# Kernel tuning notes

Measured on AMD Instinct MI355X. Metric: run time of the kernel, lower is better.

## Reference

```python
import jax, jax.numpy as jnp
import numpy as np

DECAY = 0.8
COMMITMENT = 1.0
EPS = 1e-05


def setup_inputs() -> dict:
    key = jax.random.key(0)
    k1, k2, k3 = jax.random.split(key, 3)
    dim, n_embed = 256, 8192
    input = jax.random.normal(k1, (8, 2048, dim), dtype=jnp.float32)
    embed = jax.random.normal(k2, (dim, n_embed), dtype=jnp.float32)
    cluster_size = jnp.zeros((n_embed,), dtype=jnp.float32)
    embed_avg = jax.random.normal(k3, (dim, n_embed), dtype=jnp.float32)
    return {"input": input, "embed": embed, "cluster_size": cluster_size, "embed_avg": embed_avg}


def reference(input, embed, cluster_size, embed_avg):
    dim, n_embed = embed.shape
    flatten = input.reshape(-1, dim)  # [N, d]
    dist = (jnp.sum(flatten * flatten, axis=1, keepdims=True)
            - 2.0 * flatten @ embed
            + jnp.sum(embed * embed, axis=0, keepdims=True))  # [N, C]
    embed_ind_flat = jnp.argmin(dist, axis=1)  # [N]
    embed_ind = embed_ind_flat.reshape(input.shape[:-1])
    quantize = jnp.take(embed.T, embed_ind_flat, axis=0).reshape(input.shape)

    # training-mode EMA codebook update (onehot.sum(0) and x^T @ onehot as segment ops)
    counts = jax.ops.segment_sum(jnp.ones_like(embed_ind_flat, dtype=input.dtype),
                                 embed_ind_flat, num_segments=n_embed)  # [C]
    embed_sum = jax.ops.segment_sum(flatten, embed_ind_flat, num_segments=n_embed).T  # [d, C]
    new_cluster_size = cluster_size * DECAY + counts * (1.0 - DECAY)
    new_embed_avg = embed_avg * DECAY + embed_sum * (1.0 - DECAY)
    smoothed = (new_cluster_size + EPS) / (jnp.sum(new_cluster_size) + n_embed * EPS)
    smoothed = smoothed * jnp.sum(new_cluster_size)
    new_embed = new_embed_avg / smoothed[None, :]

    commit_loss = jnp.mean((quantize - input) ** 2) * COMMITMENT
    # straight-through (no grad here in fwd-only, values identical)
    quantize_st = input + jax.lax.stop_gradient(quantize - input)
    return quantize_st, embed_ind, commit_loss, new_embed, new_cluster_size, new_embed_avg
```

## Files before the change

### kernel.cpp

```cpp
#include <hip/hip_runtime.h>
#include <hip/hip_bf16.h>
#include <float.h>
#include <stdint.h>

#define N_ROWS 16384
#define DIM 256
#define NE 8192
#define K2 768
#define DECAY 0.8f
#define OMD 0.2f
#define EPS 1e-5f
#define NPAN 8
#define NKT 24
#define NVT 96

#define WS_X2     0
#define WS_EMBEDT 0
#define WS_ESUMT  2097152
#define WS_B2T    6291456
#define WS_ENORM  9437184
#define WS_COUNTS 9445376
#define WS_SMOOTH 9453568
#define WS_PI     9592832
#define WS_LOSS   9740288
#define WS_TOTAL  9740289

#define OUT_Q    0
#define OUT_IND  4194304
#define OUT_LOSS 4210688
#define OUT_NE   4210689
#define OUT_NCS  6307841
#define OUT_NEA  6316033

typedef __attribute__((ext_vector_type(8))) short bf16x8;
typedef __attribute__((ext_vector_type(4))) float f32x4;

static __device__ __forceinline__ ushort f2bf(float f) {
    uint32_t u = __float_as_uint(f);
    uint32_t r = (u + 0x7fffu + ((u >> 16) & 1u)) >> 16;
    return (ushort)r;
}
static __device__ __forceinline__ float bf2f(ushort h) {
    return __uint_as_float(((uint32_t)h) << 16);
}
static __device__ __forceinline__ void async16(void* lds, const void* g) {
    __builtin_amdgcn_global_load_lds(
        (const __attribute__((address_space(1))) uint32_t*)g,
        (__attribute__((address_space(3))) uint32_t*)lds, 16, 0, 0);
}

__global__ __launch_bounds__(256) void convx_kernel(const float* __restrict__ x,
                                                    ushort* __restrict__ X2) {
    int i = blockIdx.x * 256 + threadIdx.x;
    int row = i >> 6, q = (i & 63) * 4;
    float4 v = *(const float4*)&x[(size_t)row * 256 + q];
    ushort4 hi, lo;
    hi.x = f2bf(v.x); hi.y = f2bf(v.y); hi.z = f2bf(v.z); hi.w = f2bf(v.w);
    lo.x = f2bf(v.x - bf2f(hi.x)); lo.y = f2bf(v.y - bf2f(hi.y));
    lo.z = f2bf(v.z - bf2f(hi.z)); lo.w = f2bf(v.w - bf2f(hi.w));
    *(ushort4*)&X2[(size_t)row * K2 + q]       = hi;
    *(ushort4*)&X2[(size_t)row * K2 + 256 + q] = lo;
    *(ushort4*)&X2[(size_t)row * K2 + 512 + q] = hi;
}

__global__ __launch_bounds__(256) void prepB_kernel(const float* __restrict__ embed,
                                                    ushort* __restrict__ B2T,
                                                    float* __restrict__ enorm) {
    __shared__ float t[32][33];
    int c0 = blockIdx.x * 32, d0 = blockIdx.y * 32;
    int tx = threadIdx.x & 31, ty = threadIdx.x >> 5;
    #pragma unroll
    for (int r = 0; r < 4; ++r)
        t[ty + r * 8][tx] = embed[(size_t)(d0 + ty + r * 8) * NE + c0 + tx];
    __syncthreads();
    #pragma unroll
    for (int r = 0; r < 4; ++r) {
        int c = c0 + ty + r * 8, d = d0 + tx;
        float v = t[tx][ty + r * 8];
        ushort hi = f2bf(v);
        ushort lo = f2bf(v - bf2f(hi));
        B2T[(size_t)c * K2 + d]       = hi;
        B2T[(size_t)c * K2 + 256 + d] = hi;
        B2T[(size_t)c * K2 + 512 + d] = lo;
        float s = v * v;
        #pragma unroll
        for (int off = 16; off; off >>= 1) s += __shfl_down(s, off, 32);
        if (tx == 0) atomicAdd(&enorm[c], s);
    }
}

__global__ __launch_bounds__(256) void transpose_kernel(const float* __restrict__ embed,
                                                        float* __restrict__ embedT) {
    __shared__ float t[32][33];
    int c0 = blockIdx.x * 32, d0 = blockIdx.y * 32;
    int tx = threadIdx.x & 31, ty = threadIdx.x >> 5;
    #pragma unroll
    for (int r = 0; r < 4; ++r)
        t[ty + r * 8][tx] = embed[(size_t)(d0 + ty + r * 8) * NE + c0 + tx];
    __syncthreads();
    #pragma unroll
    for (int r = 0; r < 4; ++r)
        embedT[(size_t)(c0 + ty + r * 8) * DIM + d0 + tx] = t[tx][ty + r * 8];
}

#define MFMA16(d, a, b) d = __builtin_amdgcn_mfma_f32_16x16x32_bf16(a, b, d, 0, 0, 0)

__global__ __launch_bounds__(1024, 4) void argmin_mfma(
    const ushort* __restrict__ X2, const ushort* __restrict__ B2T,
    const float* __restrict__ enorm, int* __restrict__ pi) {
    __shared__ ushort smem[55296];
    float* const redv = (float*)(smem + 49152);
    int*   const redc = (int*)(smem + 51200);
    float* const enS  = (float*)(smem + 53248);

    const int lin = blockIdx.x;
    const int by = lin & 7, bx = lin >> 3;
    const int row0 = bx * 256, colb = by * 1024;

    const int tid = threadIdx.x;
    const int lane = tid & 63, wid = tid >> 6;
    const int fl = lane & 15, fh = lane >> 4;
    const int wr = wid >> 2, wc = wid & 3;

    enS[tid] = enorm[colb + tid];
    redv[tid] = FLT_MAX; redc[tid] = 0x7fffffff;

    const int srow = tid >> 2;
    const int swz = (tid & 3) ^ ((tid >> 3) & 3);
    const size_t aBase = (size_t)(row0 + srow) * K2 + swz * 8;
    const size_t bBase = (size_t)(colb + srow) * K2 + swz * 8;

    async16(smem + 0 * 8192 + tid * 8, X2 + aBase);
    async16(smem + 24576 + 0 * 8192 + tid * 8, B2T + bBase);
    async16(smem + 1 * 8192 + tid * 8, X2 + aBase + 32);
    async16(smem + 24576 + 1 * 8192 + tid * 8, B2T + bBase + 32);

    const int xo = (fh ^ ((fl >> 1) & 3)) * 8;
    int aOff[4], bOff[4];
    #pragma unroll
    for (int m = 0; m < 4; ++m) aOff[m] = (wr * 64 + m * 16 + fl) * 32 + xo;
    #pragma unroll
    for (int n = 0; n < 4; ++n) bOff[n] = (wc * 64 + n * 16 + fl) * 32 + xo;

    f32x4 acc[4][4];
    #pragma unroll
    for (int m = 0; m < 4; ++m)
        #pragma unroll
        for (int n = 0; n < 4; ++n) acc[m][n] = (f32x4){0.f, 0.f, 0.f, 0.f};

    int cur = 0;
    #pragma unroll 1
    for (int vt = 0; vt < NVT; ++vt) {
        const int t = vt % NKT;
        int nv2 = vt + 2; if (nv2 >= NVT) nv2 -= NVT;
        const int nt2 = nv2 % NKT, nct2 = nv2 / NKT;
        int nbuf = cur + 2; if (nbuf >= 3) nbuf -= 3;

        async16(smem + nbuf * 8192 + tid * 8, X2 + aBase + (size_t)nt2 * 32);
        async16(smem + 24576 + nbuf * 8192 + tid * 8,
                B2T + bBase + (size_t)nct2 * 196608 + (size_t)nt2 * 32);

        asm volatile("s_waitcnt vmcnt(4)" ::: "memory");
        __builtin_amdgcn_s_barrier();
        __builtin_amdgcn_sched_barrier(0);

        const ushort* Ac = smem + cur * 8192;
        const ushort* Bc = smem + 24576 + cur * 8192;
        bf16x8 af[4], bf[4];
        #pragma unroll
        for (int n = 0; n < 4; ++n) bf[n] = *(const bf16x8*)&Bc[bOff[n]];
        #pragma unroll
        for (int m = 0; m < 4; ++m) af[m] = *(const bf16x8*)&Ac[aOff[m]];

        __builtin_amdgcn_s_setprio(1);
        #pragma unroll
        for (int m = 0; m < 4; ++m)
            #pragma unroll
            for (int n = 0; n < 4; ++n)
                MFMA16(acc[m][n], af[m], bf[n]);
        __builtin_amdgcn_s_setprio(0);

        if (t == NKT - 1) {
            const int ct = vt / NKT;
            const int cb = colb + ct * 256 + wc * 64;
            float en[4];
            #pragma unroll
            for (int n = 0; n < 4; ++n) en[n] = enS[ct * 256 + wc * 64 + n * 16 + fl];
            #pragma unroll
            for (int m = 0; m < 4; ++m)
                #pragma unroll
                for (int r = 0; r < 4; ++r) {
                    float bv = FLT_MAX; int bc = 0x7fffffff;
                    #pragma unroll
                    for (int n = 0; n < 4; ++n) {
                        float s = __builtin_fmaf(-2.f, acc[m][n][r], en[n]);
                        int c = cb + n * 16 + fl;
                        if (s < bv) { bv = s; bc = c; }
                    }
                    #pragma unroll
                    for (int off = 1; off < 16; off <<= 1) {
                        float ov = __shfl_xor(bv, off, 64);
                        int oc = __shfl_xor(bc, off, 64);
                        if (ov < bv || (ov == bv && oc < bc)) { bv = ov; bc = oc; }
                    }
                    if (fl == 0) {
                        const int slot = (wr * 64 + m * 16 + fh * 4 + r) * 4 + wc;
                        float cv = redv[slot]; int cc = redc[slot];
                        if (bv < cv || (bv == cv && bc < cc)) {
                            redv[slot] = bv; redc[slot] = bc;
                        }
                    }
                }
            #pragma unroll
            for (int m = 0; m < 4; ++m)
                #pragma unroll
                for (int n = 0; n < 4; ++n) acc[m][n] = (f32x4){0.f, 0.f, 0.f, 0.f};
        }
        __builtin_amdgcn_s_barrier();
        __builtin_amdgcn_sched_barrier(0);
        cur = cur + 1 == 3 ? 0 : cur + 1;
    }

    asm volatile("s_waitcnt vmcnt(0) lgkmcnt(0)" ::: "memory");
    __builtin_amdgcn_s_barrier();
    if (tid < 256) {
        float bv = redv[tid * 4]; int bc = redc[tid * 4];
        #pragma unroll
        for (int w = 1; w < 4; ++w) {
            float v = redv[tid * 4 + w]; int c = redc[tid * 4 + w];
            if (v < bv || (v == bv && c < bc)) { bv = v; bc = c; }
        }
        pi[(size_t)(row0 + tid) * NPAN + by] = bc;
    }
}

__global__ __launch_bounds__(256) void rerank_gather(
    const float* __restrict__ x, const float* __restrict__ embedT,
    const int* __restrict__ pi, float* __restrict__ out_ind,
    float* __restrict__ q_out, float* __restrict__ esumT,
    float* __restrict__ counts, float* __restrict__ loss_acc) {
    const int row = blockIdx.x * 4 + (threadIdx.x >> 6);
    const int lane = threadIdx.x & 63;
    float4 xv = *(const float4*)&x[(size_t)row * DIM + lane * 4];
    float bestd = FLT_MAX; int besti = 0;
    float4 ebest = {0.f, 0.f, 0.f, 0.f};
    #pragma unroll
    for (int p = 0; p < NPAN; ++p) {
        const int c = pi[(size_t)row * NPAN + p];
        float4 e = *(const float4*)&embedT[(size_t)c * DIM + lane * 4];
        float dx = e.x - xv.x, dy = e.y - xv.y, dz = e.z - xv.z, dw = e.w - xv.w;
        float s = dx * dx + dy * dy + dz * dz + dw * dw;
        #pragma unroll
        for (int off = 32; off; off >>= 1) s += __shfl_down(s, off);
        s = __shfl(s, 0);
        if (s < bestd) { bestd = s; besti = c; ebest = e; }
    }
    *(float4*)&q_out[(size_t)row * DIM + lane * 4] = ebest;
    __shared__ float ls[4];
    if (lane == 0) {
        out_ind[row] = (float)besti;
        ls[threadIdx.x >> 6] = bestd;
        atomicAdd(&counts[besti], 1.0f);
    }
    atomicAdd(&esumT[(size_t)besti * DIM + lane * 4 + 0], xv.x);
    atomicAdd(&esumT[(size_t)besti * DIM + lane * 4 + 1], xv.y);
    atomicAdd(&esumT[(size_t)besti * DIM + lane * 4 + 2], xv.z);
    atomicAdd(&esumT[(size_t)besti * DIM + lane * 4 + 3], xv.w);
    __syncthreads();
    if (threadIdx.x == 0) atomicAdd(loss_acc, ls[0] + ls[1] + ls[2] + ls[3]);
}

__global__ void ncs_kernel(const float* __restrict__ cs, const float* __restrict__ counts,
                           float* __restrict__ out_ncs, float* __restrict__ total) {
    int c = blockIdx.x * 256 + threadIdx.x;
    float v = cs[c] * DECAY + counts[c] * OMD;
    out_ncs[c] = v;
    float s = v;
    #pragma unroll
    for (int off = 32; off; off >>= 1) s += __shfl_down(s, off);
    __shared__ float bs[4];
    if ((threadIdx.x & 63) == 0) bs[threadIdx.x >> 6] = s;
    __syncthreads();
    if (threadIdx.x == 0) atomicAdd(total, bs[0] + bs[1] + bs[2] + bs[3]);
}

__global__ void smooth_kernel(const float* __restrict__ out_ncs, const float* __restrict__ total,
                              float* __restrict__ smoothed, const float* __restrict__ loss_acc,
                              float* __restrict__ out_loss) {
    int c = blockIdx.x * 256 + threadIdx.x;
    float tot = *total;
    float v = out_ncs[c];
    smoothed[c] = (v + EPS) / (tot + (float)NE * EPS) * tot;
    if (blockIdx.x == 0 && threadIdx.x == 0)
        *out_loss = *loss_acc * (1.0f / ((float)N_ROWS * (float)DIM));
}

__global__ __launch_bounds__(256) void final_kernel(
    const float* __restrict__ embed_avg, const float* __restrict__ esumT,
    const float* __restrict__ smoothed, float* __restrict__ out_ne,
    float* __restrict__ out_nea) {
    __shared__ float t[32][33];
    int c0 = blockIdx.x * 32, d0 = blockIdx.y * 32;
    int tx = threadIdx.x & 31, ty = threadIdx.x >> 5;
    #pragma unroll
    for (int r = 0; r < 4; ++r)
        t[ty + r * 8][tx] = esumT[(size_t)(c0 + ty + r * 8) * DIM + d0 + tx];
    __syncthreads();
    #pragma unroll
    for (int r = 0; r < 4; ++r) {
        int d = d0 + ty + r * 8, c = c0 + tx;
        float es = t[tx][ty + r * 8];
        float ea = embed_avg[(size_t)d * NE + c] * DECAY + es * OMD;
        out_nea[(size_t)d * NE + c] = ea;
        out_ne[(size_t)d * NE + c] = ea / smoothed[c];
    }
}

extern "C" void kernel_launch(void* const* d_in, const int* in_sizes, int n_in,
                              void* d_out, int out_size, void* d_ws, size_t ws_size,
                              hipStream_t stream) {
    const float* input     = (const float*)d_in[0];
    const float* embed     = (const float*)d_in[1];
    const float* cs        = (const float*)d_in[2];
    const float* embed_avg = (const float*)d_in[3];
    float* out = (float*)d_out;
    float* ws  = (float*)d_ws;

    hipMemsetAsync(ws + WS_COUNTS, 0, (size_t)8192 * 4, stream);
    hipMemsetAsync(ws + WS_ENORM, 0, (size_t)8192 * 4, stream);
    hipMemsetAsync(ws + WS_LOSS, 0, (size_t)2 * 4, stream);

    convx_kernel<<<4096, 256, 0, stream>>>(input, (ushort*)(ws + WS_X2));
    prepB_kernel<<<dim3(256, 8), 256, 0, stream>>>(embed, (ushort*)(ws + WS_B2T),
                                                   ws + WS_ENORM);
    argmin_mfma<<<512, 1024, 0, stream>>>(
        (const ushort*)(ws + WS_X2), (const ushort*)(ws + WS_B2T), ws + WS_ENORM,
        (int*)(ws + WS_PI));
    transpose_kernel<<<dim3(256, 8), 256, 0, stream>>>(embed, ws + WS_EMBEDT);
    hipMemsetAsync(ws + WS_ESUMT, 0, (size_t)2097152 * 4, stream);
    rerank_gather<<<4096, 256, 0, stream>>>(input, ws + WS_EMBEDT, (int*)(ws + WS_PI),
                                            out + OUT_IND, out + OUT_Q,
                                            ws + WS_ESUMT, ws + WS_COUNTS, ws + WS_LOSS);
    ncs_kernel<<<32, 256, 0, stream>>>(cs, ws + WS_COUNTS, out + OUT_NCS, ws + WS_TOTAL);
    smooth_kernel<<<32, 256, 0, stream>>>(out + OUT_NCS, ws + WS_TOTAL, ws + WS_SMOOTH,
                                          ws + WS_LOSS, out + OUT_LOSS);
    final_kernel<<<dim3(256, 8), 256, 0, stream>>>(embed_avg, ws + WS_ESUMT, ws + WS_SMOOTH,
                                                   out + OUT_NE, out + OUT_NEA);
}
```

Baseline: 461.0 us.

## Split argmin GEMM per 256-column tile across blocks, merge via 64-bit atomicMin

Each argmin block now handles a single 256x256 output tile instead of looping over four column tiles, so the grid is four times larger. Per-panel partial minima are combined across blocks with a packed (order-preserving float key, index) 64-bit atomicMin into a workspace array that is pre-filled with 0xFF. The pipeline drops from triple to double buffering, shared memory shrinks, and the launch bound changes to 2 blocks per CU. This is meant to raise parallelism and occupancy and to remove the in-loop epilogue branch, at the cost of global atomics, an extra memset and a shallower prefetch.

```diff
diff --git a/kernel.cpp b/kernel.cpp
--- a/kernel.cpp
+++ b/kernel.cpp
@@ -11,8 +11,7 @@
 #define OMD 0.2f
 #define EPS 1e-5f
 #define NPAN 8
-#define NKT 24
-#define NVT 96
+#define NVT 24
 
 #define WS_X2     0
 #define WS_EMBEDT 0
@@ -21,7 +20,7 @@
 #define WS_ENORM  9437184
 #define WS_COUNTS 9445376
 #define WS_SMOOTH 9453568
-#define WS_PI     9592832
+#define WS_PV64   9461760
 #define WS_LOSS   9740288
 #define WS_TOTAL  9740289
 
@@ -105,24 +104,27 @@
 
 #define MFMA16(d, a, b) d = __builtin_amdgcn_mfma_f32_16x16x32_bf16(a, b, d, 0, 0, 0)
 
-__global__ __launch_bounds__(1024, 4) void argmin_mfma(
+__global__ __launch_bounds__(1024, 2) void argmin_mfma(
     const ushort* __restrict__ X2, const ushort* __restrict__ B2T,
-    const float* __restrict__ enorm, int* __restrict__ pi) {
-    __shared__ ushort smem[55296];
-    float* const redv = (float*)(smem + 49152);
-    int*   const redc = (int*)(smem + 51200);
-    float* const enS  = (float*)(smem + 53248);
+    const float* __restrict__ enorm, unsigned long long* __restrict__ pv64) {
+    __shared__ ushort smem[37376];
+    float* const redv = (float*)(smem + 32768);
+    int*   const redc = (int*)(smem + 34816);
+    float* const enS  = (float*)(smem + 36864);
 
     const int lin = blockIdx.x;
-    const int by = lin & 7, bx = lin >> 3;
-    const int row0 = bx * 256, colb = by * 1024;
+    const int xcd = lin & 7, q = lin >> 3;
+    const int rb = q & 7, ct = q >> 3;
+    const int row0 = (xcd * 8 + rb) * 256;
+    const int colb = ct * 256;
+    const int panel = ct >> 2;
 
     const int tid = threadIdx.x;
     const int lane = tid & 63, wid = tid >> 6;
     const int fl = lane & 15, fh = lane >> 4;
     const int wr = wid >> 2, wc = wid & 3;
 
-    enS[tid] = enorm[colb + tid];
+    if (tid < 256) enS[tid] = enorm[colb + tid];
     redv[tid] = FLT_MAX; redc[tid] = 0x7fffffff;
 
     const int srow = tid >> 2;
@@ -131,9 +133,7 @@
     const size_t bBase = (size_t)(colb + srow) * K2 + swz * 8;
 
     async16(smem + 0 * 8192 + tid * 8, X2 + aBase);
-    async16(smem + 24576 + 0 * 8192 + tid * 8, B2T + bBase);
-    async16(smem + 1 * 8192 + tid * 8, X2 + aBase + 32);
-    async16(smem + 24576 + 1 * 8192 + tid * 8, B2T + bBase + 32);
+    async16(smem + 16384 + 0 * 8192 + tid * 8, B2T + bBase);
 
     const int xo = (fh ^ ((fl >> 1) & 3)) * 8;
     int aOff[4], bOff[4];
@@ -148,24 +148,20 @@
         #pragma unroll
         for (int n = 0; n < 4; ++n) acc[m][n] = (f32x4){0.f, 0.f, 0.f, 0.f};
 
-    int cur = 0;
     #pragma unroll 1
     for (int vt = 0; vt < NVT; ++vt) {
-        const int t = vt % NKT;
-        int nv2 = vt + 2; if (nv2 >= NVT) nv2 -= NVT;
-        const int nt2 = nv2 % NKT, nct2 = nv2 / NKT;
-        int nbuf = cur + 2; if (nbuf >= 3) nbuf -= 3;
-
-        async16(smem + nbuf * 8192 + tid * 8, X2 + aBase + (size_t)nt2 * 32);
-        async16(smem + 24576 + nbuf * 8192 + tid * 8,
-                B2T + bBase + (size_t)nct2 * 196608 + (size_t)nt2 * 32);
-
-        asm volatile("s_waitcnt vmcnt(4)" ::: "memory");
+        int nv = vt + 1; if (nv == NVT) nv = 0;
+        const int nbuf = nv & 1, cbuf = vt & 1;
+
+        async16(smem + nbuf * 8192 + tid * 8, X2 + aBase + (size_t)nv * 32);
+        async16(smem + 16384 + nbuf * 8192 + tid * 8, B2T + bBase + (size_t)nv * 32);
+
+        asm volatile("s_waitcnt vmcnt(2)" ::: "memory");
         __builtin_amdgcn_s_barrier();
         __builtin_amdgcn_sched_barrier(0);
 
-        const ushort* Ac = smem + cur * 8192;
-        const ushort* Bc = smem + 24576 + cur * 8192;
+        const ushort* Ac = smem + cbuf * 8192;
+        const ushort* Bc = smem + 16384 + cbuf * 8192;
         bf16x8 af[4], bf[4];
         #pragma unroll
         for (int n = 0; n < 4; ++n) bf[n] = *(const bf16x8*)&Bc[bOff[n]];
@@ -180,49 +176,36 @@
                 MFMA16(acc[m][n], af[m], bf[n]);
         __builtin_amdgcn_s_setprio(0);
 
-        if (t == NKT - 1) {
-            const int ct = vt / NKT;
-            const int cb = colb + ct * 256 + wc * 64;
-            float en[4];
-            #pragma unroll
-            for (int n = 0; n < 4; ++n) en[n] = enS[ct * 256 + wc * 64 + n * 16 + fl];
-            #pragma unroll
-            for (int m = 0; m < 4; ++m)
-                #pragma unroll
-                for (int r = 0; r < 4; ++r) {
-                    float bv = FLT_MAX; int bc = 0x7fffffff;
-                    #pragma unroll
-                    for (int n = 0; n < 4; ++n) {
-                        float s = __builtin_fmaf(-2.f, acc[m][n][r], en[n]);
-                        int c = cb + n * 16 + fl;
-                        if (s < bv) { bv = s; bc = c; }
-                    }
-                    #pragma unroll
-                    for (int off = 1; off < 16; off <<= 1) {
-                        float ov = __shfl_xor(bv, off, 64);
-                        int oc = __shfl_xor(bc, off, 64);
-                        if (ov < bv || (ov == bv && oc < bc)) { bv = ov; bc = oc; }
-                    }
-                    if (fl == 0) {
-                        const int slot = (wr * 64 + m * 16 + fh * 4 + r) * 4 + wc;
-                        float cv = redv[slot]; int cc = redc[slot];
-                        if (bv < cv || (bv == cv && bc < cc)) {
-                            redv[slot] = bv; redc[slot] = bc;
-                        }
-                    }
-                }
-            #pragma unroll
-            for (int m = 0; m < 4; ++m)
-                #pragma unroll
-                for (int n = 0; n < 4; ++n) acc[m][n] = (f32x4){0.f, 0.f, 0.f, 0.f};
-        }
         __builtin_amdgcn_s_barrier();
         __builtin_amdgcn_sched_barrier(0);
-        cur = cur + 1 == 3 ? 0 : cur + 1;
-    }
-
-    asm volatile("s_waitcnt vmcnt(0) lgkmcnt(0)" ::: "memory");
-    __builtin_amdgcn_s_barrier();
+    }
+
+    float en[4];
+    #pragma unroll
+    for (int n = 0; n < 4; ++n) en[n] = enS[wc * 64 + n * 16 + fl];
+    #pragma unroll
+    for (int m = 0; m < 4; ++m)
+        #pragma unroll
+        for (int r = 0; r < 4; ++r) {
+            float bv = FLT_MAX; int bc = 0x7fffffff;
+            #pragma unroll
+            for (int n = 0; n < 4; ++n) {
+                float s = __builtin_fmaf(-2.f, acc[m][n][r], en[n]);
+                int c = colb + wc * 64 + n * 16 + fl;
+                if (s < bv) { bv = s; bc = c; }
+            }
+            #pragma unroll
+            for (int off = 1; off < 16; off <<= 1) {
+                float ov = __shfl_xor(bv, off, 64);
+                int oc = __shfl_xor(bc, off, 64);
+                if (ov < bv || (ov == bv && oc < bc)) { bv = ov; bc = oc; }
+            }
+            if (fl == 0) {
+                const int slot = (wr * 64 + m * 16 + fh * 4 + r) * 4 + wc;
+                redv[slot] = bv; redc[slot] = bc;
+            }
+        }
+    __syncthreads();
     if (tid < 256) {
         float bv = redv[tid * 4]; int bc = redc[tid * 4];
         #pragma unroll
@@ -230,13 +213,16 @@
             float v = redv[tid * 4 + w]; int c = redc[tid * 4 + w];
             if (v < bv || (v == bv && c < bc)) { bv = v; bc = c; }
         }
-        pi[(size_t)(row0 + tid) * NPAN + by] = bc;
+        unsigned int u = __float_as_uint(bv);
+        unsigned int key = (u & 0x80000000u) ? ~u : (u | 0x80000000u);
+        unsigned long long pk = ((unsigned long long)key << 32) | (unsigned int)bc;
+        atomicMin(&pv64[(size_t)(row0 + tid) * NPAN + panel], pk);
     }
 }
 
 __global__ __launch_bounds__(256) void rerank_gather(
     const float* __restrict__ x, const float* __restrict__ embedT,
-    const int* __restrict__ pi, float* __restrict__ out_ind,
+    const unsigned long long* __restrict__ pv64, float* __restrict__ out_ind,
     float* __restrict__ q_out, float* __restrict__ esumT,
     float* __restrict__ counts, float* __restrict__ loss_acc) {
     const int row = blockIdx.x * 4 + (threadIdx.x >> 6);
@@ -246,7 +232,7 @@
     float4 ebest = {0.f, 0.f, 0.f, 0.f};
     #pragma unroll
     for (int p = 0; p < NPAN; ++p) {
-        const int c = pi[(size_t)row * NPAN + p];
+        const int c = (int)(unsigned int)(pv64[(size_t)row * NPAN + p] & 0xffffffffull);
         float4 e = *(const float4*)&embedT[(size_t)c * DIM + lane * 4];
         float dx = e.x - xv.x, dy = e.y - xv.y, dz = e.z - xv.z, dw = e.w - xv.w;
         float s = dx * dx + dy * dy + dz * dz + dw * dw;
@@ -329,16 +315,18 @@
     hipMemsetAsync(ws + WS_COUNTS, 0, (size_t)8192 * 4, stream);
     hipMemsetAsync(ws + WS_ENORM, 0, (size_t)8192 * 4, stream);
     hipMemsetAsync(ws + WS_LOSS, 0, (size_t)2 * 4, stream);
+    hipMemsetAsync(ws + WS_PV64, 0xFF, (size_t)16384 * NPAN * 8, stream);
 
     convx_kernel<<<4096, 256, 0, stream>>>(input, (ushort*)(ws + WS_X2));
     prepB_kernel<<<dim3(256, 8), 256, 0, stream>>>(embed, (ushort*)(ws + WS_B2T),
                                                    ws + WS_ENORM);
-    argmin_mfma<<<512, 1024, 0, stream>>>(
+    argmin_mfma<<<2048, 1024, 0, stream>>>(
         (const ushort*)(ws + WS_X2), (const ushort*)(ws + WS_B2T), ws + WS_ENORM,
-        (int*)(ws + WS_PI));
+        (unsigned long long*)(ws + WS_PV64));
     transpose_kernel<<<dim3(256, 8), 256, 0, stream>>>(embed, ws + WS_EMBEDT);
     hipMemsetAsync(ws + WS_ESUMT, 0, (size_t)2097152 * 4, stream);
-    rerank_gather<<<4096, 256, 0, stream>>>(input, ws + WS_EMBEDT, (int*)(ws + WS_PI),
+    rerank_gather<<<4096, 256, 0, stream>>>(input, ws + WS_EMBEDT,
+                                            (const unsigned long long*)(ws + WS_PV64),
                                             out + OUT_IND, out + OUT_Q,
                                             ws + WS_ESUMT, ws + WS_COUNTS, ws + WS_LOSS);
     ncs_kernel<<<32, 256, 0, stream>>>(cs, ws + WS_COUNTS, out + OUT_NCS, ws + WS_TOTAL);
```

After: 422.6 us. 8.3% less time.
